# Performance work log

Measured on AMD Instinct MI355X. Metric: run time of the kernel, lower is better.

The kernel has to match this reference:

```python
import jax, jax.numpy as jnp
import numpy as np

NUM_HEADS = 32
NUM_KV_HEADS = 8
HEAD_SIZE = 128
BLOCK_SIZE = 16
T = 16384                 # number of tokens (decode step, batch_size tokens)
NUM_SLOTS = 32768         # num_blocks * block_size
ROPE_BASE = 10000.0
MAX_POS = 4096


def _rope_neox(x, cos, sin):
    # x: [T, H, head_size]; cos/sin: [T, 1, head_size//2]
    d = x.shape[-1] // 2
    x1, x2 = x[..., :d], x[..., d:]
    return jnp.concatenate([x1 * cos - x2 * sin, x2 * cos + x1 * sin], axis=-1)


def setup_inputs() -> dict:
    key = jax.random.key(0)
    kq, kk, kv, kp, ks = jax.random.split(key, 5)
    q = jax.random.normal(kq, (T, NUM_HEADS * HEAD_SIZE), dtype=jnp.float32)
    k = jax.random.normal(kk, (T, NUM_KV_HEADS * HEAD_SIZE), dtype=jnp.float32)
    v = jax.random.normal(kv, (T, NUM_KV_HEADS * HEAD_SIZE), dtype=jnp.float32)
    positions = jax.random.randint(kp, (T,), 0, MAX_POS, dtype=jnp.int32)
    # unique slots (paged cache: each token gets its own slot)
    slot_mapping = jax.random.permutation(ks, NUM_SLOTS)[:T].astype(jnp.int32)
    k_cache = jnp.zeros((NUM_SLOTS, NUM_KV_HEADS, HEAD_SIZE), dtype=jnp.float32)
    v_cache = jnp.zeros((NUM_SLOTS, NUM_KV_HEADS, HEAD_SIZE), dtype=jnp.float32)
    return {"q": q, "k": k, "v": v, "positions": positions,
            "slot_mapping": slot_mapping, "k_cache": k_cache, "v_cache": v_cache}


def reference(q, k, v, positions, slot_mapping, k_cache, v_cache):
    n = q.shape[0]
    q = q.reshape(n, NUM_HEADS, HEAD_SIZE)
    k = k.reshape(n, NUM_KV_HEADS, HEAD_SIZE)
    v = v.reshape(n, NUM_KV_HEADS, HEAD_SIZE)
    # rotary frequencies (neox style, rotary_dim == head_size)
    inv_freq = 1.0 / (ROPE_BASE ** (jnp.arange(0, HEAD_SIZE, 2, dtype=jnp.float32) / HEAD_SIZE))
    freqs = positions.astype(jnp.float32)[:, None] * inv_freq  # [T, head_size//2]
    cos = jnp.cos(freqs)[:, None, :]
    sin = jnp.sin(freqs)[:, None, :]
    q_rot = _rope_neox(q, cos, sin)
    k_rot = _rope_neox(k, cos, sin)
    # paged KV-cache scatter write (unified_kv_cache_update)
    k_cache_new = k_cache.at[slot_mapping].set(k_rot)
    v_cache_new = v_cache.at[slot_mapping].set(v)
    return q_rot, k_rot, v, k_cache_new, v_cache_new
```

## Files before the change

kernel.cpp:

```cpp
#include <hip/hip_runtime.h>
#include <math.h>

constexpr int NUM_HEADS    = 32;
constexpr int NUM_KV_HEADS = 8;
constexpr int HEAD_SIZE    = 128;
constexpr int T            = 16384;
constexpr int NUM_SLOTS    = 32768;
constexpr int QD = NUM_HEADS * HEAD_SIZE;
constexpr int KD = NUM_KV_HEADS * HEAD_SIZE;
constexpr int HALF = HEAD_SIZE / 2;

constexpr size_t Q_OUT  = 0;
constexpr size_t K_OUT  = (size_t)T * QD;
constexpr size_t V_OUT  = K_OUT + (size_t)T * KD;
constexpr size_t KC_OUT = V_OUT + (size_t)T * KD;
constexpr size_t VC_OUT = KC_OUT + (size_t)NUM_SLOTS * KD;

__device__ __forceinline__ void rope4(const float4& a, const float4& b,
                                      const float* cs, const float* sn, int j0,
                                      float4& o1, float4& o2) {
    o1.x = a.x * cs[j0 + 0] - b.x * sn[j0 + 0];
    o1.y = a.y * cs[j0 + 1] - b.y * sn[j0 + 1];
    o1.z = a.z * cs[j0 + 2] - b.z * sn[j0 + 2];
    o1.w = a.w * cs[j0 + 3] - b.w * sn[j0 + 3];
    o2.x = b.x * cs[j0 + 0] + a.x * sn[j0 + 0];
    o2.y = b.y * cs[j0 + 1] + a.y * sn[j0 + 1];
    o2.z = b.z * cs[j0 + 2] + a.z * sn[j0 + 2];
    o2.w = b.w * cs[j0 + 3] + a.w * sn[j0 + 3];
}

__global__ __launch_bounds__(256) void mark_slots_kernel(
    const int* __restrict__ slot_mapping, int* __restrict__ mapped)
{
    const int i = blockIdx.x * 256 + threadIdx.x;
    if (i < T) mapped[slot_mapping[i]] = 1;
}

__global__ __launch_bounds__(256) void cache_fill_kernel(
    const float* __restrict__ k_cache, const float* __restrict__ v_cache,
    const int* __restrict__ mapped, float* __restrict__ out)
{
    const int slot = blockIdx.x;
    if (mapped[slot]) return;
    const int tid = threadIdx.x;
    const size_t row = (size_t)slot * KD;
    const float4 kv = ((const float4*)(k_cache + row))[tid];
    const float4 vv = ((const float4*)(v_cache + row))[tid];
    ((float4*)(out + KC_OUT + row))[tid] = kv;
    ((float4*)(out + VC_OUT + row))[tid] = vv;
}

__global__ __launch_bounds__(256) void rope_kv_kernel(
    const float* __restrict__ q, const float* __restrict__ k,
    const float* __restrict__ v,
    const int* __restrict__ positions, const int* __restrict__ slot_mapping,
    float* __restrict__ out)
{
    const int tok = blockIdx.x;
    const int tid = threadIdx.x;

    __shared__ float cs[HALF];
    __shared__ float sn[HALF];

    const int pos  = positions[tok];
    const int slot = slot_mapping[tok];

    if (tid < HALF) {
        const double inv = exp(-(double)(2 * tid) * (log(10000.0) / 128.0));
        const float freq = (float)((double)pos * inv);
        float s, c;
        sincosf(freq, &s, &c);
        cs[tid] = c;
        sn[tid] = s;
    }
    __syncthreads();

    {
        const float4* qrow = (const float4*)(q + (size_t)tok * QD);
        float4*       orow = (float4*)(out + Q_OUT + (size_t)tok * QD);
        #pragma unroll
        for (int i = 0; i < 2; ++i) {
            const int p    = i * 256 + tid;
            const int head = p >> 4;
            const int jq   = p & 15;
            const int j0   = jq * 4;
            const float4 a = qrow[head * 32 + jq];
            const float4 b = qrow[head * 32 + 16 + jq];
            float4 o1, o2;
            rope4(a, b, cs, sn, j0, o1, o2);
            orow[head * 32 + jq]      = o1;
            orow[head * 32 + 16 + jq] = o2;
        }
    }

    if (tid < 128) {
        const int head = tid >> 4;
        const int jq   = tid & 15;
        const int j0   = jq * 4;
        const float4* krow = (const float4*)(k + (size_t)tok * KD);
        const float4 a = krow[head * 32 + jq];
        const float4 b = krow[head * 32 + 16 + jq];
        float4 o1, o2;
        rope4(a, b, cs, sn, j0, o1, o2);
        float4* korow = (float4*)(out + K_OUT + (size_t)tok * KD);
        korow[head * 32 + jq]      = o1;
        korow[head * 32 + 16 + jq] = o2;
        float4* kcrow = (float4*)(out + KC_OUT + (size_t)slot * KD);
        kcrow[head * 32 + jq]      = o1;
        kcrow[head * 32 + 16 + jq] = o2;
    }

    {
        const float4* vrow = (const float4*)(v + (size_t)tok * KD);
        const float4 val = vrow[tid];
        ((float4*)(out + V_OUT  + (size_t)tok  * KD))[tid] = val;
        ((float4*)(out + VC_OUT + (size_t)slot * KD))[tid] = val;
    }
}

extern "C" void kernel_launch(void* const* d_in, const int* in_sizes, int n_in,
                              void* d_out, int out_size, void* d_ws, size_t ws_size,
                              hipStream_t stream) {
    const float* q   = (const float*)d_in[0];
    const float* k   = (const float*)d_in[1];
    const float* v   = (const float*)d_in[2];
    const int* positions    = (const int*)d_in[3];
    const int* slot_mapping = (const int*)d_in[4];
    const float* k_cache = (const float*)d_in[5];
    const float* v_cache = (const float*)d_in[6];
    float* out = (float*)d_out;
    int* mapped = (int*)d_ws;

    hipMemsetAsync(mapped, 0, (size_t)NUM_SLOTS * sizeof(int), stream);
    mark_slots_kernel<<<(T + 255) / 256, 256, 0, stream>>>(slot_mapping, mapped);
    cache_fill_kernel<<<NUM_SLOTS, 256, 0, stream>>>(k_cache, v_cache, mapped, out);
    rope_kv_kernel<<<T, 256, 0, stream>>>(q, k, v, positions, slot_mapping, out);
}
```

Before: 240.5 us.

## Fuse cache-fill and rope kernels into one launch with nontemporal memory ops

Merges the cache-fill kernel and the rope/KV kernel into a single grid where the first T blocks do rope and the remaining blocks copy unmapped cache slots. This removes one kernel launch and lets the two independent streams of work overlap across the GPU. All global loads and stores now use nontemporal builtins so the streaming traffic bypasses cache retention. The risk is that mixing block types makes the load uneven across the grid, and that the nontemporal hints could hurt if the hardware handles them poorly.

```diff
diff --git a/kernel.cpp b/kernel.cpp
--- a/kernel.cpp
+++ b/kernel.cpp
@@ -16,9 +16,18 @@
 constexpr size_t KC_OUT = V_OUT + (size_t)T * KD;
 constexpr size_t VC_OUT = KC_OUT + (size_t)NUM_SLOTS * KD;
 
-__device__ __forceinline__ void rope4(const float4& a, const float4& b,
+typedef float f4 __attribute__((ext_vector_type(4)));
+
+__device__ __forceinline__ f4 ntload4(const float* p) {
+    return __builtin_nontemporal_load((const f4*)p);
+}
+__device__ __forceinline__ void ntstore4(float* p, f4 v) {
+    __builtin_nontemporal_store(v, (f4*)p);
+}
+
+__device__ __forceinline__ void rope4(const f4 a, const f4 b,
                                       const float* cs, const float* sn, int j0,
-                                      float4& o1, float4& o2) {
+                                      f4& o1, f4& o2) {
     o1.x = a.x * cs[j0 + 0] - b.x * sn[j0 + 0];
     o1.y = a.y * cs[j0 + 1] - b.y * sn[j0 + 1];
     o1.z = a.z * cs[j0 + 2] - b.z * sn[j0 + 2];
@@ -36,28 +45,28 @@
     if (i < T) mapped[slot_mapping[i]] = 1;
 }
 
-__global__ __launch_bounds__(256) void cache_fill_kernel(
+__global__ __launch_bounds__(256) void fused_rope_fill_kernel(
+    const float* __restrict__ q, const float* __restrict__ k,
+    const float* __restrict__ v,
+    const int* __restrict__ positions, const int* __restrict__ slot_mapping,
     const float* __restrict__ k_cache, const float* __restrict__ v_cache,
     const int* __restrict__ mapped, float* __restrict__ out)
 {
-    const int slot = blockIdx.x;
-    if (mapped[slot]) return;
+    const int b   = blockIdx.x;
     const int tid = threadIdx.x;
-    const size_t row = (size_t)slot * KD;
-    const float4 kv = ((const float4*)(k_cache + row))[tid];
-    const float4 vv = ((const float4*)(v_cache + row))[tid];
-    ((float4*)(out + KC_OUT + row))[tid] = kv;
-    ((float4*)(out + VC_OUT + row))[tid] = vv;
-}
 
-__global__ __launch_bounds__(256) void rope_kv_kernel(
-    const float* __restrict__ q, const float* __restrict__ k,
-    const float* __restrict__ v,
-    const int* __restrict__ positions, const int* __restrict__ slot_mapping,
-    float* __restrict__ out)
-{
-    const int tok = blockIdx.x;
-    const int tid = threadIdx.x;
+    if (b >= T) {
+        const int slot = b - T;
+        if (mapped[slot]) return;
+        const size_t row = (size_t)slot * KD;
+        const f4 kv = ntload4(k_cache + row + tid * 4);
+        const f4 vv = ntload4(v_cache + row + tid * 4);
+        ntstore4(out + KC_OUT + row + tid * 4, kv);
+        ntstore4(out + VC_OUT + row + tid * 4, vv);
+        return;
+    }
+
+    const int tok = b;
 
     __shared__ float cs[HALF];
     __shared__ float sn[HALF];
@@ -76,20 +85,20 @@
     __syncthreads();
 
     {
-        const float4* qrow = (const float4*)(q + (size_t)tok * QD);
-        float4*       orow = (float4*)(out + Q_OUT + (size_t)tok * QD);
+        const float* qrow = q + (size_t)tok * QD;
+        float*       orow = out + Q_OUT + (size_t)tok * QD;
         #pragma unroll
         for (int i = 0; i < 2; ++i) {
             const int p    = i * 256 + tid;
             const int head = p >> 4;
             const int jq   = p & 15;
             const int j0   = jq * 4;
-            const float4 a = qrow[head * 32 + jq];
-            const float4 b = qrow[head * 32 + 16 + jq];
-            float4 o1, o2;
-            rope4(a, b, cs, sn, j0, o1, o2);
-            orow[head * 32 + jq]      = o1;
-            orow[head * 32 + 16 + jq] = o2;
+            const f4 a  = ntload4(qrow + head * 128 + j0);
+            const f4 bq = ntload4(qrow + head * 128 + 64 + j0);
+            f4 o1, o2;
+            rope4(a, bq, cs, sn, j0, o1, o2);
+            ntstore4(orow + head * 128 + j0,      o1);
+            ntstore4(orow + head * 128 + 64 + j0, o2);
         }
     }
 
@@ -97,24 +106,23 @@
         const int head = tid >> 4;
         const int jq   = tid & 15;
         const int j0   = jq * 4;
-        const float4* krow = (const float4*)(k + (size_t)tok * KD);
-        const float4 a = krow[head * 32 + jq];
-        const float4 b = krow[head * 32 + 16 + jq];
-        float4 o1, o2;
-        rope4(a, b, cs, sn, j0, o1, o2);
-        float4* korow = (float4*)(out + K_OUT + (size_t)tok * KD);
-        korow[head * 32 + jq]      = o1;
-        korow[head * 32 + 16 + jq] = o2;
-        float4* kcrow = (float4*)(out + KC_OUT + (size_t)slot * KD);
-        kcrow[head * 32 + jq]      = o1;
-        kcrow[head * 32 + 16 + jq] = o2;
+        const float* krow = k + (size_t)tok * KD;
+        const f4 a  = ntload4(krow + head * 128 + j0);
+        const f4 bk = ntload4(krow + head * 128 + 64 + j0);
+        f4 o1, o2;
+        rope4(a, bk, cs, sn, j0, o1, o2);
+        float* korow = out + K_OUT + (size_t)tok * KD;
+        ntstore4(korow + head * 128 + j0,      o1);
+        ntstore4(korow + head * 128 + 64 + j0, o2);
+        float* kcrow = out + KC_OUT + (size_t)slot * KD;
+        ntstore4(kcrow + head * 128 + j0,      o1);
+        ntstore4(kcrow + head * 128 + 64 + j0, o2);
     }
 
     {
-        const float4* vrow = (const float4*)(v + (size_t)tok * KD);
-        const float4 val = vrow[tid];
-        ((float4*)(out + V_OUT  + (size_t)tok  * KD))[tid] = val;
-        ((float4*)(out + VC_OUT + (size_t)slot * KD))[tid] = val;
+        const f4 val = ntload4(v + (size_t)tok * KD + tid * 4);
+        ntstore4(out + V_OUT  + (size_t)tok  * KD + tid * 4, val);
+        ntstore4(out + VC_OUT + (size_t)slot * KD + tid * 4, val);
     }
 }
 
@@ -131,8 +139,8 @@
     float* out = (float*)d_out;
     int* mapped = (int*)d_ws;
 
-    hipMemsetAsync(mapped, 0, (size_t)NUM_SLOTS * sizeof(int), stream);
+    (void)hipMemsetAsync(mapped, 0, (size_t)NUM_SLOTS * sizeof(int), stream);
     mark_slots_kernel<<<(T + 255) / 256, 256, 0, stream>>>(slot_mapping, mapped);
-    cache_fill_kernel<<<NUM_SLOTS, 256, 0, stream>>>(k_cache, v_cache, mapped, out);
-    rope_kv_kernel<<<T, 256, 0, stream>>>(q, k, v, positions, slot_mapping, out);
+    fused_rope_fill_kernel<<<T + NUM_SLOTS, 256, 0, stream>>>(
+        q, k, v, positions, slot_mapping, k_cache, v_cache, mapped, out);
 }
```

After: 216.4 us. 1.11x faster.
